# Kernel tuning notes

Hardware: AMD Instinct MI355X
Metric: run time of the kernel (lower is better)

Reference implementation:

```python
import jax, jax.numpy as jnp
import numpy as np

B, T, D, E = 4, 8192, 2048, 64


def setup_inputs() -> dict:
    key = jax.random.key(0)
    k1, k2 = jax.random.split(key)
    x = jax.random.normal(k1, (B, T, D), dtype=jnp.float32)
    kernel_DE = jax.random.normal(k2, (D, E), dtype=jnp.float32) * 0.02
    return {"x": x, "kernel_DE": kernel_DE, "num_experts_per_tok": 8}


def reference(x, kernel_DE, num_experts_per_tok):
    dtype = x.dtype
    # router logits: (B,T,E)
    router_logits_BTE = jnp.einsum("BTD,DE->BTE", x, kernel_DE)
    # gating probs in fp32 for numerical stability
    activated_gating_BTE = jax.nn.softmax(router_logits_BTE.astype(jnp.float32), axis=-1)
    # top-k experts per token
    weights_BTX, selected_experts_BTX = jax.lax.top_k(activated_gating_BTE, num_experts_per_tok)
    # renormalize selected weights via softmax in model dtype (faithful to source)
    normalized_weights_BTX = jax.nn.softmax(weights_BTX.astype(dtype), axis=-1)
    return (normalized_weights_BTX, selected_experts_BTX)
```

## Files before the change

### kernel.cpp

```cpp
#include <hip/hip_runtime.h>
#include <math.h>

#define NTOK  32768
#define DDIM  2048
#define NEXP  64
#define TOPK  8
#define GAP_THR  1e-4f
#define LIST_CAP 16384

#define WFRAG_OFF  1024
#define WFRAG_SZ   (64 * 4 * 2048)
#define LIST_OFF   (WFRAG_OFF + WFRAG_SZ)

#define NKS   32

typedef __attribute__((ext_vector_type(8))) short s8_t;
typedef __attribute__((ext_vector_type(4))) float f4_t;
typedef __attribute__((ext_vector_type(4))) unsigned int u4_t;

typedef const __attribute__((address_space(1))) unsigned int* as1p;
typedef __attribute__((address_space(3))) unsigned int* as3p;

__device__ __forceinline__ void gl2lds16(const void* g, void* l) {
  __builtin_amdgcn_global_load_lds((as1p)g, (as3p)l, 16, 0, 0);
}

__device__ __forceinline__ unsigned short f2bf(float f) {
  const unsigned u = __builtin_bit_cast(unsigned, f);
  const unsigned r = u + 0x7FFFu + ((u >> 16) & 1u);
  return (unsigned short)(r >> 16);
}

struct bfpair { unsigned hi, lo; };
__device__ __forceinline__ bfpair split2(float a, float b) {
  const unsigned ua = __builtin_bit_cast(unsigned, a);
  const unsigned ub = __builtin_bit_cast(unsigned, b);
  const unsigned ra = ua + 0x7FFFu + ((ua >> 16) & 1u);
  const unsigned rb = ub + 0x7FFFu + ((ub >> 16) & 1u);
  bfpair r;
  r.hi = (ra >> 16) | (rb & 0xFFFF0000u);
  const float fa = a - __builtin_bit_cast(float, ra & 0xFFFF0000u);
  const float fb = b - __builtin_bit_cast(float, rb & 0xFFFF0000u);
  r.lo = (__builtin_bit_cast(unsigned, fa) >> 16) |
         (__builtin_bit_cast(unsigned, fb) & 0xFFFF0000u);
  return r;
}

__global__ void wprep(const float* __restrict__ w, unsigned short* __restrict__ wf,
                      int* __restrict__ cnt) {
  if (blockIdx.x == 0 && threadIdx.x == 0) cnt[0] = 0;
  const int ks   = blockIdx.x;
  const int eg   = threadIdx.x >> 6;
  const int lane = threadIdx.x & 63;
  const int kb   = ks * 32 + ((lane >> 4) << 3);
  const int e    = (eg << 4) + (lane & 15);
  s8_t h, l;
#pragma unroll
  for (int j = 0; j < 8; ++j) {
    const float v = w[(size_t)(kb + j) * NEXP + e];
    const unsigned short hb = f2bf(v);
    const float hf = __builtin_bit_cast(float, (unsigned)hb << 16);
    h[j] = (short)hb;
    l[j] = (short)f2bf(v - hf);
  }
  unsigned short* base = wf + (size_t)(ks * 4 + eg) * 1024 + lane * 8;
  *(s8_t*)(base)       = h;
  *(s8_t*)(base + 512) = l;
}

__global__ __launch_bounds__(512, 4) void router_main(
    const float* __restrict__ x, const unsigned short* __restrict__ wfg,
    float* __restrict__ out, int* __restrict__ cnt, int* __restrict__ list) {
  __shared__ union {
    struct {
      float xb[2][8][512];
      unsigned short wb[2][2][4096];
    } s;
    float ll[64 * 68];
  } u;

  const int tid  = threadIdx.x;
  const int lane = tid & 63;
  const int wave = tid >> 6;
  const int pair = wave & 3;
  const int half = wave >> 2;
  const int col  = lane & 15;
  const int kgrp = lane >> 4;
  const int tok0 = blockIdx.x * 64 + pair * 16;

  f4_t acc[4];
#pragma unroll
  for (int eg = 0; eg < 4; ++eg) acc[eg] = (f4_t){0.f, 0.f, 0.f, 0.f};

  const float* gx = x + (size_t)(tok0 + col) * DDIM + half * (NKS * 32) + (kgrp << 3);
  const unsigned short* gw0 = wfg + pair * 1024 + lane * 8;

  auto issue = [&](int j, int bb) {
    gl2lds16(gx + j * 32,     &u.s.xb[bb][wave][0]);
    gl2lds16(gx + j * 32 + 4, &u.s.xb[bb][wave][256]);
    const unsigned short* g = gw0 + (size_t)(half * NKS + j) * 4096;
    gl2lds16(g,       &u.s.wb[bb][half][pair * 1024]);
    gl2lds16(g + 512, &u.s.wb[bb][half][pair * 1024 + 512]);
  };

  auto compute = [&](int bb) {
    const float* lx = &u.s.xb[bb][wave][0];
    const unsigned short* lw = &u.s.wb[bb][half][0];
    const float4 v0 = *(const float4*)(lx + lane * 4);
    const float4 v1 = *(const float4*)(lx + 256 + lane * 4);
    const bfpair p0 = split2(v0.x, v0.y);
    const bfpair p1 = split2(v0.z, v0.w);
    const bfpair p2 = split2(v1.x, v1.y);
    const bfpair p3 = split2(v1.z, v1.w);
    const u4_t uh = {p0.hi, p1.hi, p2.hi, p3.hi};
    const u4_t ul = {p0.lo, p1.lo, p2.lo, p3.lo};
    const s8_t ah = __builtin_bit_cast(s8_t, uh);
    const s8_t al = __builtin_bit_cast(s8_t, ul);
#pragma unroll
    for (int eg = 0; eg < 4; ++eg) {
      const s8_t bh = *(const s8_t*)(lw + eg * 1024 + lane * 8);
      const s8_t bl = *(const s8_t*)(lw + eg * 1024 + 512 + lane * 8);
      acc[eg] = __builtin_amdgcn_mfma_f32_16x16x32_bf16(ah, bh, acc[eg], 0, 0, 0);
      acc[eg] = __builtin_amdgcn_mfma_f32_16x16x32_bf16(al, bh, acc[eg], 0, 0, 0);
      acc[eg] = __builtin_amdgcn_mfma_f32_16x16x32_bf16(ah, bl, acc[eg], 0, 0, 0);
    }
  };

  issue(0, 0);

#pragma unroll 1
  for (int c = 0; c < NKS - 1; ++c) {
    issue(c + 1, (c + 1) & 1);
    asm volatile("s_waitcnt vmcnt(4)" ::: "memory");
    __builtin_amdgcn_s_barrier();
    asm volatile("" ::: "memory");
    compute(c & 1);
    asm volatile("" ::: "memory");
    __builtin_amdgcn_s_barrier();
  }
  asm volatile("s_waitcnt vmcnt(0)" ::: "memory");
  __builtin_amdgcn_s_barrier();
  asm volatile("" ::: "memory");
  compute((NKS - 1) & 1);
  __syncthreads();

  if (half == 0) {
#pragma unroll
    for (int eg = 0; eg < 4; ++eg)
#pragma unroll
      for (int r = 0; r < 4; ++r)
        u.ll[(pair * 16 + kgrp * 4 + r) * 68 + eg * 16 + col] = acc[eg][r];
  }
  __syncthreads();
  if (half == 1) {
#pragma unroll
    for (int eg = 0; eg < 4; ++eg)
#pragma unroll
      for (int r = 0; r < 4; ++r)
        u.ll[(pair * 16 + kgrp * 4 + r) * 68 + eg * 16 + col] += acc[eg][r];
  }
  __syncthreads();

  float* out_w = out;
  float* out_i = out + (size_t)NTOK * TOPK;

  const int trow0 = pair * 16 + half * 8;
#pragma unroll 1
  for (int t = 0; t < 8; ++t) {
    const int row = trow0 + t;
    const int tok = blockIdx.x * 64 + row;
    const float v = u.ll[row * 68 + lane];

    float m = v;
#pragma unroll
    for (int off = 32; off; off >>= 1) m = fmaxf(m, __shfl_xor(m, off));
    const float ex = __expf(v - m);
    float s = ex;
#pragma unroll
    for (int off = 32; off; off >>= 1) s += __shfl_xor(s, off);
    float pw = ex / s;
    float lw = v;
    int   ii = lane;

    float selp[TOPK + 1];
    float sell[TOPK + 1];
    int   seli[TOPK + 1];
#pragma unroll
    for (int r = 0; r < TOPK + 1; ++r) {
      float bp = pw; float bl = lw; int bi = ii;
#pragma unroll
      for (int off = 32; off; off >>= 1) {
        const float op = __shfl_xor(bp, off);
        const float ol = __shfl_xor(bl, off);
        const int   oi = __shfl_xor(bi, off);
        const bool take = (op > bp) || (op == bp && oi < bi);
        bp = take ? op : bp;
        bl = take ? ol : bl;
        bi = take ? oi : bi;
      }
      selp[r] = bp; sell[r] = bl; seli[r] = bi;
      if (lane == bi) pw = -__builtin_inff();
    }

    bool contested = false;
#pragma unroll
    for (int k = 0; k < TOPK; ++k)
      contested |= (sell[k] - sell[k + 1]) <= GAP_THR;

    const float mm = selp[0];
    float ssum = 0.0f;
#pragma unroll
    for (int k = 0; k < TOPK; ++k) ssum += __expf(selp[k] - mm);
    float myv = selp[0];
    int   myi = seli[0];
#pragma unroll
    for (int k = 1; k < TOPK; ++k)
      if (lane == k) { myv = selp[k]; myi = seli[k]; }
    if (lane < TOPK) {
      out_w[(size_t)tok * TOPK + lane] = __expf(myv - mm) / ssum;
      out_i[(size_t)tok * TOPK + lane] = (float)myi;
    }

    if (contested && lane == 0) {
      const int idx = atomicAdd(cnt, 1);
      if (idx < LIST_CAP) list[idx] = tok;
    }
  }
}

__global__ __launch_bounds__(256, 1) void router_fix(
    const float* __restrict__ x, const float* __restrict__ w,
    float* __restrict__ out, const int* __restrict__ cnt,
    const int* __restrict__ list) {
  const int lane = threadIdx.x & 63;
  const int wave = threadIdx.x >> 6;
  const int gw   = blockIdx.x * 4 + wave;
  const int NW   = gridDim.x * 4;

  int n = cnt[0];
  if (n > LIST_CAP) n = LIST_CAP;

  float* out_w = out;
  float* out_i = out + (size_t)NTOK * TOPK;

  for (int i = gw; i < n; i += NW) {
    const int tok = list[i];
    const float* xr = x + (size_t)tok * DDIM;
    double a0 = 0.0, a1 = 0.0, a2 = 0.0, a3 = 0.0;
#pragma unroll 4
    for (int d4 = 0; d4 < DDIM / 4; ++d4) {
      const float4 xv = *(const float4*)(xr + d4 * 4);
      const int r = d4 * 4;
      a0 = fma((double)xv.x, (double)w[(r + 0) * NEXP + lane], a0);
      a1 = fma((double)xv.y, (double)w[(r + 1) * NEXP + lane], a1);
      a2 = fma((double)xv.z, (double)w[(r + 2) * NEXP + lane], a2);
      a3 = fma((double)xv.w, (double)w[(r + 3) * NEXP + lane], a3);
    }
    const double a = (a0 + a1) + (a2 + a3);

    double dm = a;
#pragma unroll
    for (int off = 32; off; off >>= 1) dm = fmax(dm, __shfl_xor(dm, off));
    const double dex = exp(a - dm);
    double ds = dex;
#pragma unroll
    for (int off = 32; off; off >>= 1) ds += __shfl_xor(ds, off);
    double dpv = dex / ds;

    double dselv[TOPK];
    int    dseli[TOPK];
#pragma unroll
    for (int r = 0; r < TOPK; ++r) {
      double bv = dpv;
      int    bi = lane;
#pragma unroll
      for (int off = 32; off; off >>= 1) {
        const double ov = __shfl_xor(bv, off);
        const int    oi = __shfl_xor(bi, off);
        const bool take = (ov > bv) || (ov == bv && oi < bi);
        bv = take ? ov : bv;
        bi = take ? oi : bi;
      }
      dselv[r] = bv;
      dseli[r] = bi;
      if (lane == bi) dpv = -1.0e300;
    }
    const double dmm = dselv[0];
    double dssum = 0.0;
#pragma unroll
    for (int k = 0; k < TOPK; ++k) dssum += exp(dselv[k] - dmm);
    double myv = dselv[0];
    int    myi = dseli[0];
#pragma unroll
    for (int k = 1; k < TOPK; ++k)
      if (lane == k) { myv = dselv[k]; myi = dseli[k]; }
    if (lane < TOPK) {
      out_w[(size_t)tok * TOPK + lane] = (float)(exp(myv - dmm) / dssum);
      out_i[(size_t)tok * TOPK + lane] = (float)myi;
    }
  }
}

extern "C" void kernel_launch(void* const* d_in, const int* in_sizes, int n_in,
                              void* d_out, int out_size, void* d_ws, size_t ws_size,
                              hipStream_t stream) {
  const float* x = (const float*)d_in[0];
  const float* w = (const float*)d_in[1];
  int* cnt = (int*)d_ws;
  unsigned short* wfrag = (unsigned short*)((char*)d_ws + WFRAG_OFF);
  int* list = (int*)((char*)d_ws + LIST_OFF);

  wprep<<<dim3(64), dim3(256), 0, stream>>>(w, wfrag, cnt);
  router_main<<<dim3(NTOK / 64), dim3(512), 0, stream>>>(
      x, wfrag, (float*)d_out, cnt, list);
  router_fix<<<dim3(256), dim3(256), 0, stream>>>(
      x, w, (float*)d_out, cnt, list);
}
```

Before: 529.1 us.

## Give each wave its own 16-token tile over full K, doubling tokens per block

Each block now handles 128 tokens, and each of its 8 waves owns 16 tokens across the full D dimension. This replaces the old scheme where wave pairs split K in halves and summed partials through shared memory. The weight fragment tile in LDS is shared by all 8 waves, which halves weight traffic per token. The x tile uses an XOR-swizzled layout to avoid LDS bank conflicts. The cost is 64 sequential K steps instead of 32, with fewer loads per step, and lower occupancy (launch bounds 2 instead of 4), which may leave less latency hiding for this memory-bound read of x.

Measured after the change: 539.2 us. No clear change (+1.9%).

```diff
diff --git a/kernel.cpp b/kernel.cpp
--- a/kernel.cpp
+++ b/kernel.cpp
@@ -12,7 +12,8 @@
 #define WFRAG_SZ   (64 * 4 * 2048)
 #define LIST_OFF   (WFRAG_OFF + WFRAG_SZ)
 
-#define NKS   32
+#define NKS   64
+#define TOKB  128
 
 typedef __attribute__((ext_vector_type(8))) short s8_t;
 typedef __attribute__((ext_vector_type(4))) float f4_t;
@@ -68,46 +69,46 @@
   *(s8_t*)(base + 512) = l;
 }
 
-__global__ __launch_bounds__(512, 4) void router_main(
+__global__ __launch_bounds__(512, 2) void router_main(
     const float* __restrict__ x, const unsigned short* __restrict__ wfg,
     float* __restrict__ out, int* __restrict__ cnt, int* __restrict__ list) {
-  __shared__ union {
-    struct {
-      float xb[2][8][512];
-      unsigned short wb[2][2][4096];
-    } s;
-    float ll[64 * 68];
+  __shared__ union __align__(16) {
+    char ring[2][24 * 1024];
+    float ll[TOKB * 68];
   } u;
 
   const int tid  = threadIdx.x;
   const int lane = tid & 63;
   const int wave = tid >> 6;
-  const int pair = wave & 3;
-  const int half = wave >> 2;
   const int col  = lane & 15;
   const int kgrp = lane >> 4;
-  const int tok0 = blockIdx.x * 64 + pair * 16;
+  const int wtok = blockIdx.x * TOKB + wave * 16;
 
   f4_t acc[4];
 #pragma unroll
   for (int eg = 0; eg < 4; ++eg) acc[eg] = (f4_t){0.f, 0.f, 0.f, 0.f};
 
-  const float* gx = x + (size_t)(tok0 + col) * DDIM + half * (NKS * 32) + (kgrp << 3);
-  const unsigned short* gw0 = wfg + pair * 1024 + lane * 8;
-
-  auto issue = [&](int j, int bb) {
-    gl2lds16(gx + j * 32,     &u.s.xb[bb][wave][0]);
-    gl2lds16(gx + j * 32 + 4, &u.s.xb[bb][wave][256]);
-    const unsigned short* g = gw0 + (size_t)(half * NKS + j) * 4096;
-    gl2lds16(g,       &u.s.wb[bb][half][pair * 1024]);
-    gl2lds16(g + 512, &u.s.wb[bb][half][pair * 1024 + 512]);
+  const int r8l = lane >> 3;
+  const int s8l = lane & 7;
+  const float* gx0 = x + (size_t)(wtok + r8l) * DDIM + ((s8l ^ r8l) << 2);
+  const float* gx1 = gx0 + (size_t)8 * DDIM;
+  const char*  gwb = (const char*)wfg + wave * 1024 + lane * 16;
+
+  auto issue = [&](int c) {
+    const int s = c & 1;
+    char* xb = u.ring[s] + wave * 2048;
+    gl2lds16(gx0 + c * 32, xb);
+    gl2lds16(gx1 + c * 32, xb + 1024);
+    gl2lds16(gwb + (size_t)c * 8192, u.ring[s] + 16384 + wave * 1024);
   };
 
-  auto compute = [&](int bb) {
-    const float* lx = &u.s.xb[bb][wave][0];
-    const unsigned short* lw = &u.s.wb[bb][half][0];
-    const float4 v0 = *(const float4*)(lx + lane * 4);
-    const float4 v1 = *(const float4*)(lx + 256 + lane * 4);
+  auto compute = [&](int c) {
+    const int s = c & 1;
+    const char* lxb = u.ring[s] + wave * 2048;
+    const char* lwb = u.ring[s] + 16384;
+    const int q  = (col >> 3) * 1024 + (col & 7) * 128;
+    const float4 v0 = *(const float4*)(lxb + q + (((2 * kgrp)     ^ (col & 7)) << 4));
+    const float4 v1 = *(const float4*)(lxb + q + (((2 * kgrp + 1) ^ (col & 7)) << 4));
     const bfpair p0 = split2(v0.x, v0.y);
     const bfpair p1 = split2(v0.z, v0.w);
     const bfpair p2 = split2(v1.x, v1.y);
@@ -118,57 +119,46 @@
     const s8_t al = __builtin_bit_cast(s8_t, ul);
 #pragma unroll
     for (int eg = 0; eg < 4; ++eg) {
-      const s8_t bh = *(const s8_t*)(lw + eg * 1024 + lane * 8);
-      const s8_t bl = *(const s8_t*)(lw + eg * 1024 + 512 + lane * 8);
+      const s8_t bh = *(const s8_t*)(lwb + eg * 2048 + lane * 16);
+      const s8_t bl = *(const s8_t*)(lwb + eg * 2048 + 1024 + lane * 16);
       acc[eg] = __builtin_amdgcn_mfma_f32_16x16x32_bf16(ah, bh, acc[eg], 0, 0, 0);
       acc[eg] = __builtin_amdgcn_mfma_f32_16x16x32_bf16(al, bh, acc[eg], 0, 0, 0);
       acc[eg] = __builtin_amdgcn_mfma_f32_16x16x32_bf16(ah, bl, acc[eg], 0, 0, 0);
     }
   };
 
-  issue(0, 0);
+  issue(0);
 
 #pragma unroll 1
   for (int c = 0; c < NKS - 1; ++c) {
-    issue(c + 1, (c + 1) & 1);
-    asm volatile("s_waitcnt vmcnt(4)" ::: "memory");
+    issue(c + 1);
+    asm volatile("s_waitcnt vmcnt(3)" ::: "memory");
     __builtin_amdgcn_s_barrier();
     asm volatile("" ::: "memory");
-    compute(c & 1);
+    compute(c);
     asm volatile("" ::: "memory");
     __builtin_amdgcn_s_barrier();
   }
   asm volatile("s_waitcnt vmcnt(0)" ::: "memory");
   __builtin_amdgcn_s_barrier();
   asm volatile("" ::: "memory");
-  compute((NKS - 1) & 1);
+  compute(NKS - 1);
   __syncthreads();
 
-  if (half == 0) {
-#pragma unroll
-    for (int eg = 0; eg < 4; ++eg)
-#pragma unroll
-      for (int r = 0; r < 4; ++r)
-        u.ll[(pair * 16 + kgrp * 4 + r) * 68 + eg * 16 + col] = acc[eg][r];
-  }
-  __syncthreads();
-  if (half == 1) {
-#pragma unroll
-    for (int eg = 0; eg < 4; ++eg)
-#pragma unroll
-      for (int r = 0; r < 4; ++r)
-        u.ll[(pair * 16 + kgrp * 4 + r) * 68 + eg * 16 + col] += acc[eg][r];
-  }
+#pragma unroll
+  for (int eg = 0; eg < 4; ++eg)
+#pragma unroll
+    for (int r = 0; r < 4; ++r)
+      u.ll[(wave * 16 + kgrp * 4 + r) * 68 + eg * 16 + col] = acc[eg][r];
   __syncthreads();
 
   float* out_w = out;
   float* out_i = out + (size_t)NTOK * TOPK;
 
-  const int trow0 = pair * 16 + half * 8;
 #pragma unroll 1
-  for (int t = 0; t < 8; ++t) {
-    const int row = trow0 + t;
-    const int tok = blockIdx.x * 64 + row;
+  for (int t = 0; t < 16; ++t) {
+    const int row = wave * 16 + t;
+    const int tok = blockIdx.x * TOKB + row;
     const float v = u.ll[row * 68 + lane];
 
     float m = v;
@@ -311,7 +301,7 @@
   int* list = (int*)((char*)d_ws + LIST_OFF);
 
   wprep<<<dim3(64), dim3(256), 0, stream>>>(w, wfrag, cnt);
-  router_main<<<dim3(NTOK / 64), dim3(512), 0, stream>>>(
+  router_main<<<dim3(NTOK / TOKB), dim3(512), 0, stream>>>(
       x, wfrag, (float*)d_out, cnt, list);
   router_fix<<<dim3(256), dim3(256), 0, stream>>>(
       x, w, (float*)d_out, cnt, list);
```
